# Kernel tuning notes

Measured on AMD Instinct MI355X. Metric: run time of the kernel, lower is better.

Reference implementation:

```python
import jax, jax.numpy as jnp
import numpy as np

N, E, F_IN, ED, G, LAT = 50000, 800000, 16, 4, 500, 32
HID = 64
EPS = 1e-5
NEG = 0.2


def _gat(x, src, dst, ea, W, a_s, a_d, We, a_e, bias, heads, ch):
    n = x.shape[0]
    h = (x @ W).reshape(n, heads, ch)                      # [N,H,C]
    he = (ea @ We).reshape(-1, heads, ch)                  # [E,H,C]
    asrc = jnp.sum(h * a_s, -1)                            # [N,H]
    adst = jnp.sum(h * a_d, -1)                            # [N,H]
    ae = jnp.sum(he * a_e, -1)                             # [E,H]
    alpha = jax.nn.leaky_relu(asrc[src] + adst[dst] + ae, NEG)
    amax = jax.ops.segment_max(alpha, dst, num_segments=n)
    amax = jnp.where(jnp.isfinite(amax), amax, 0.0)
    ealpha = jnp.exp(alpha - amax[dst])
    denom = jax.ops.segment_sum(ealpha, dst, num_segments=n)
    coef = ealpha / (denom[dst] + 1e-16)                   # [E,H]
    msg = h[src] * coef[:, :, None]                        # [E,H,C]
    out = jax.ops.segment_sum(msg, dst, num_segments=n)
    return out.reshape(n, heads * ch) + bias


def _bn(x, g, b):
    mu = x.mean(0)
    var = x.var(0)
    return g * (x - mu) * jax.lax.rsqrt(var + EPS) + b


def setup_inputs():
    key = jax.random.key(0)
    ks = jax.random.split(key, 20)
    d = {}
    d['x'] = jax.random.normal(ks[0], (N, F_IN), jnp.float32)
    d['edge_index'] = jax.random.randint(ks[1], (2, E), 0, N, jnp.int32)
    d['edge_attr'] = jax.random.normal(ks[2], (E, ED), jnp.float32)
    d['batch'] = jnp.sort(jax.random.randint(ks[3], (N,), 0, G, jnp.int32))
    d['W1'] = jax.random.normal(ks[4], (F_IN, 3 * HID), jnp.float32) / np.sqrt(F_IN)
    d['a1s'] = jax.random.normal(ks[5], (3, HID), jnp.float32) / np.sqrt(HID)
    d['a1d'] = jax.random.normal(ks[6], (3, HID), jnp.float32) / np.sqrt(HID)
    d['We1'] = jax.random.normal(ks[7], (ED, 3 * HID), jnp.float32) / np.sqrt(ED)
    d['a1e'] = jax.random.normal(ks[8], (3, HID), jnp.float32) / np.sqrt(HID)
    d['b1'] = jnp.zeros((3 * HID,), jnp.float32)
    d['g1'] = jnp.ones((3 * HID,), jnp.float32)
    d['be1'] = jnp.zeros((3 * HID,), jnp.float32)
    d['W2'] = jax.random.normal(ks[9], (3 * HID, HID), jnp.float32) / np.sqrt(3 * HID)
    d['a2s'] = jax.random.normal(ks[10], (1, HID), jnp.float32) / np.sqrt(HID)
    d['a2d'] = jax.random.normal(ks[11], (1, HID), jnp.float32) / np.sqrt(HID)
    d['We2'] = jax.random.normal(ks[12], (ED, HID), jnp.float32) / np.sqrt(ED)
    d['a2e'] = jax.random.normal(ks[13], (1, HID), jnp.float32) / np.sqrt(HID)
    d['b2'] = jnp.zeros((HID,), jnp.float32)
    d['g2'] = jnp.ones((HID,), jnp.float32)
    d['be2'] = jnp.zeros((HID,), jnp.float32)
    d['wA'] = jax.random.normal(ks[14], (HID, 1), jnp.float32) / np.sqrt(HID)
    d['bA'] = jnp.zeros((1,), jnp.float32)
    d['wMu'] = jax.random.normal(ks[15], (HID, LAT), jnp.float32) / np.sqrt(HID)
    d['bMu'] = jnp.zeros((LAT,), jnp.float32)
    d['wLv'] = jax.random.normal(ks[16], (HID, LAT), jnp.float32) / np.sqrt(HID)
    d['bLv'] = jnp.zeros((LAT,), jnp.float32)
    return d


def reference(x, edge_index, edge_attr, batch, W1, a1s, a1d, We1, a1e, b1, g1, be1,
              W2, a2s, a2d, We2, a2e, b2, g2, be2, wA, bA, wMu, bMu, wLv, bLv):
    src, dst = edge_index[0], edge_index[1]
    h1 = _gat(x, src, dst, edge_attr, W1, a1s, a1d, We1, a1e, b1, 3, HID)
    h1 = _bn(jax.nn.elu(h1), g1, be1)
    h2 = _gat(h1, src, dst, edge_attr, W2, a2s, a2d, We2, a2e, b2, 1, HID)
    h2 = _bn(jax.nn.elu(h2), g2, be2)
    gate = jax.nn.sigmoid(h2 @ wA + bA)                    # [N,1]
    h2 = h2 * gate
    hg = jax.ops.segment_sum(h2, batch, num_segments=G)    # [G,HID]
    return hg @ wMu + bMu, hg @ wLv + bLv
```

## Files before the change

kernel.cpp:

```cpp
#include <hip/hip_runtime.h>
#include <math.h>

#define N_NODES 50000
#define N_EDGES 800000
#define FIN     16
#define EDIM    4
#define NGRAPH  500
#define LATD    32
#define HID     64
#define C1      192
#define H1      3
#define EPS_BN  1e-5f
#define NEGSL   0.2f
#define ROWS1   128
#define ROWS2   128
#define PAD2    196

__device__ __forceinline__ float wred(float v) {
    #pragma unroll
    for (int o = 32; o > 0; o >>= 1) v += __shfl_xor(v, o, 64);
    return v;
}
__device__ __forceinline__ float wmax(float v) {
    #pragma unroll
    for (int o = 32; o > 0; o >>= 1) v = fmaxf(v, __shfl_xor(v, o, 64));
    return v;
}

__global__ void k_v(const float* __restrict__ We1, const float* __restrict__ a1e,
                    const float* __restrict__ We2, const float* __restrict__ a2e,
                    float* __restrict__ V) {
    int t = threadIdx.x;
    if (t < 12) {
        int k = t / 3, h = t % 3;
        float s = 0.f;
        for (int c = 0; c < HID; ++c) s += We1[k*C1 + h*HID + c] * a1e[h*HID + c];
        V[k*3 + h] = s;
    } else if (t < 16) {
        int k = t - 12;
        float s = 0.f;
        for (int c = 0; c < HID; ++c) s += We2[k*HID + c] * a2e[c];
        V[12 + k] = s;
    }
}

__global__ void k_h1att(const float* __restrict__ x, const float* __restrict__ W1,
                        const float* __restrict__ a1s, const float* __restrict__ a1d,
                        float* __restrict__ h1, float* __restrict__ asrc,
                        float* __restrict__ adst) {
    int w = blockIdx.x * (blockDim.x >> 6) + (threadIdx.x >> 6);
    int lane = threadIdx.x & 63;
    if (w >= N_NODES * H1) return;
    int n = w / H1, h = w % H1;
    int c = h*HID + lane;
    const float* xr = x + n * FIN;
    float acc = 0.f;
    #pragma unroll
    for (int k = 0; k < FIN; ++k) acc += xr[k] * W1[k*C1 + c];
    h1[n*C1 + c] = acc;
    float s = wred(acc * a1s[c]);
    float d = wred(acc * a1d[c]);
    if (lane == 0) { asrc[n*H1 + h] = s; adst[n*H1 + h] = d; }
}

__global__ void k_deg(const int* __restrict__ ei, int* __restrict__ deg) {
    int e = blockIdx.x * blockDim.x + threadIdx.x;
    if (e >= N_EDGES) return;
    atomicAdd(&deg[ei[N_EDGES + e]], 1);
}

__global__ void k_scan(const int* __restrict__ deg, int* __restrict__ row,
                       int* __restrict__ cur) {
    __shared__ int part[1024];
    const int T = 1024, CH = 52;
    int t = threadIdx.x;
    int base = t * CH;
    int s = 0;
    if (base < N_NODES) {
        int hi = min(base + CH, N_NODES);
        int i = base;
        for (; i + 3 < hi; i += 4) { int4 v = *(const int4*)(deg + i); s += v.x + v.y + v.z + v.w; }
        for (; i < hi; ++i) s += deg[i];
    }
    part[t] = s;
    __syncthreads();
    for (int off = 1; off < T; off <<= 1) {
        int v = (t >= off) ? part[t - off] : 0;
        __syncthreads();
        part[t] += v;
        __syncthreads();
    }
    int run = (t == 0) ? 0 : part[t - 1];
    if (base <= N_NODES) {
        int hi = min(base + CH, N_NODES + 1);
        for (int i = base; i < hi; ++i) {
            row[i] = run;
            if (i < N_NODES) { cur[i] = run; run += deg[i]; }
        }
    }
}

__global__ void k_perm(const int* __restrict__ ei, int* __restrict__ cur,
                       int* __restrict__ eperm) {
    int e = blockIdx.x * blockDim.x + threadIdx.x;
    if (e >= N_EDGES) return;
    int d = ei[N_EDGES + e];
    int j = atomicAdd(&cur[d], 1);
    eperm[j] = e;
}

__global__ void k_fill2(const int* __restrict__ ei, const float* __restrict__ ea,
                        const int* __restrict__ eperm,
                        const float* __restrict__ asrc, const float* __restrict__ adst,
                        const float* __restrict__ V,
                        int* __restrict__ srcp, int* __restrict__ dstp,
                        float* __restrict__ alpha1, float* __restrict__ ae2) {
    int j = blockIdx.x * blockDim.x + threadIdx.x;
    if (j >= N_EDGES) return;
    int e = eperm[j];
    int s = ei[e], d = ei[N_EDGES + e];
    srcp[j] = s;
    dstp[j] = d;
    float4 ev = ((const float4*)ea)[e];
    ae2[j] = ev.x*V[12] + ev.y*V[13] + ev.z*V[14] + ev.w*V[15];
    #pragma unroll
    for (int h = 0; h < H1; ++h) {
        float a = asrc[s*H1 + h] + adst[d*H1 + h]
                + ev.x*V[h] + ev.y*V[3+h] + ev.z*V[6+h] + ev.w*V[9+h];
        a = a > 0.f ? a : NEGSL * a;
        alpha1[(size_t)h*N_EDGES + j] = a;
    }
}

__global__ void k_agg1(const int* __restrict__ row, const int* __restrict__ srcp,
                       const float* __restrict__ alpha, const float* __restrict__ h1,
                       float* __restrict__ out1) {
    __shared__ int2 pairs[4][64];
    int wid = threadIdx.x >> 6;
    int lane = threadIdx.x & 63;
    int w = blockIdx.x * 4 + wid;
    if (w >= N_NODES * H1) return;
    int d = w / H1, h = w % H1;
    int r0 = row[d], r1 = row[d + 1];
    const float* ap = alpha + (size_t)h*N_EDGES;

    float m = -1e30f;
    for (int j = r0 + lane; j < r1; j += 64) m = fmaxf(m, ap[j]);
    m = wmax(m);

    float ssum = 0.f;
    for (int j = r0 + lane; j < r1; j += 64) ssum += __expf(ap[j] - m);
    ssum = wred(ssum);
    float inv = 1.f / (ssum + 1e-16f);

    int slot = lane >> 4, c4 = lane & 15;
    const float* hbase = h1 + h*HID + c4*4;
    float4 acc = make_float4(0.f, 0.f, 0.f, 0.f);
    for (int base = r0; base < r1; base += 64) {
        int n = min(64, r1 - base);
        if (lane < n) {
            float cf = __expf(ap[base + lane] - m) * inv;
            pairs[wid][lane] = make_int2(srcp[base + lane], __float_as_int(cf));
        }
        #pragma unroll 4
        for (int idx = slot; idx < n; idx += 4) {
            int2 p = pairs[wid][idx];
            float cf = __int_as_float(p.y);
            const float4 hv = *(const float4*)(hbase + (size_t)p.x * C1);
            acc.x += cf * hv.x; acc.y += cf * hv.y;
            acc.z += cf * hv.z; acc.w += cf * hv.w;
        }
    }
    #pragma unroll
    for (int o = 16; o < 64; o <<= 1) {
        acc.x += __shfl_xor(acc.x, o, 64);
        acc.y += __shfl_xor(acc.y, o, 64);
        acc.z += __shfl_xor(acc.z, o, 64);
        acc.w += __shfl_xor(acc.w, o, 64);
    }
    if (lane < 16)
        *(float4*)(out1 + (size_t)d*C1 + h*HID + c4*4) = acc;
}

__global__ void k_stats1(float* __restrict__ out, const float* __restrict__ b,
                         float* __restrict__ stats) {
    int c = threadIdx.x;
    int r0 = blockIdx.x * ROWS1;
    int r1 = min(r0 + ROWS1, N_NODES);
    float bc = b[c];
    float s = 0.f, ss = 0.f;
    for (int r = r0; r < r1; ++r) {
        float v = out[r*C1 + c] + bc;
        v = v > 0.f ? v : expm1f(v);
        out[r*C1 + c] = v;
        s += v; ss += v * v;
    }
    atomicAdd(&stats[c], s);
    atomicAdd(&stats[C1 + c], ss);
}

__global__ void k_fin1(float* __restrict__ stats) {
    int c = threadIdx.x;
    if (c < C1) {
        float mu  = stats[c] / (float)N_NODES;
        float var = stats[C1 + c] / (float)N_NODES - mu * mu;
        stats[2*C1 + c] = mu;
        stats[3*C1 + c] = rsqrtf(var + EPS_BN);
    }
}

__global__ void k_norm1(float* __restrict__ out, const float* __restrict__ g,
                        const float* __restrict__ be, const float* __restrict__ stats) {
    int i = blockIdx.x * blockDim.x + threadIdx.x;
    if (i >= N_NODES * C1) return;
    int c = i % C1;
    out[i] = g[c] * (out[i] - stats[2*C1 + c]) * stats[3*C1 + c] + be[c];
}

__global__ void __launch_bounds__(256) k_h2(
        const float* __restrict__ h1bn, const float* __restrict__ W2,
        const float* __restrict__ a2s, const float* __restrict__ a2d,
        float* __restrict__ h2, float* __restrict__ asrc, float* __restrict__ adst) {
    __shared__ float As[64 * PAD2];
    int tid = threadIdx.x;
    int nb = blockIdx.x * 64;
    const float4* src = (const float4*)(h1bn + (size_t)nb * C1);
    #pragma unroll
    for (int j = 0; j < 12; ++j) {
        int idx = tid + j * 256;
        int n = idx / 48, kq = idx - n * 48;
        *(float4*)(As + n * PAD2 + kq * 4) = src[idx];
    }
    __syncthreads();

    int lane = tid & 63;
    int tx = lane & 15, tyw = lane >> 4;
    int ty = (tid >> 6) * 4 + tyw;
    int r0 = ty * 4;
    const float* wp = W2 + tx * 4;

    float4 acc0 = {0,0,0,0}, acc1 = {0,0,0,0}, acc2 = {0,0,0,0}, acc3 = {0,0,0,0};
    #pragma unroll 4
    for (int k = 0; k < C1; ++k) {
        float4 w4 = *(const float4*)(wp + k * HID);
        float a0 = As[(r0+0)*PAD2 + k];
        float a1 = As[(r0+1)*PAD2 + k];
        float a2 = As[(r0+2)*PAD2 + k];
        float a3 = As[(r0+3)*PAD2 + k];
        acc0.x += a0*w4.x; acc0.y += a0*w4.y; acc0.z += a0*w4.z; acc0.w += a0*w4.w;
        acc1.x += a1*w4.x; acc1.y += a1*w4.y; acc1.z += a1*w4.z; acc1.w += a1*w4.w;
        acc2.x += a2*w4.x; acc2.y += a2*w4.y; acc2.z += a2*w4.z; acc2.w += a2*w4.w;
        acc3.x += a3*w4.x; acc3.y += a3*w4.y; acc3.z += a3*w4.z; acc3.w += a3*w4.w;
    }

    float4 s4 = *(const float4*)(a2s + tx*4);
    float4 d4 = *(const float4*)(a2d + tx*4);

    #define H2_EPI(ACC, I)                                                        \
    {                                                                             \
        int n = nb + r0 + (I);                                                    \
        float s = ACC.x*s4.x + ACC.y*s4.y + ACC.z*s4.z + ACC.w*s4.w;              \
        float d = ACC.x*d4.x + ACC.y*d4.y + ACC.z*d4.z + ACC.w*d4.w;              \
        s += __shfl_xor(s, 1, 64); s += __shfl_xor(s, 2, 64);                     \
        s += __shfl_xor(s, 4, 64); s += __shfl_xor(s, 8, 64);                     \
        d += __shfl_xor(d, 1, 64); d += __shfl_xor(d, 2, 64);                     \
        d += __shfl_xor(d, 4, 64); d += __shfl_xor(d, 8, 64);                     \
        if (n < N_NODES) {                                                        \
            *(float4*)(h2 + (size_t)n*HID + tx*4) = ACC;                          \
            if (tx == 0) { asrc[n] = s; adst[n] = d; }                            \
        }                                                                         \
    }
    H2_EPI(acc0, 0)
    H2_EPI(acc1, 1)
    H2_EPI(acc2, 2)
    H2_EPI(acc3, 3)
    #undef H2_EPI
}

__global__ void k_alpha2(const int* __restrict__ srcp, const int* __restrict__ dstp,
                         const float* __restrict__ ae2,
                         const float* __restrict__ asrc, const float* __restrict__ adst,
                         float* __restrict__ alpha2) {
    int j = blockIdx.x * blockDim.x + threadIdx.x;
    if (j >= N_EDGES) return;
    float a = asrc[srcp[j]] + adst[dstp[j]] + ae2[j];
    a = a > 0.f ? a : NEGSL * a;
    alpha2[j] = a;
}

__global__ void k_agg2(const int* __restrict__ row, const int* __restrict__ srcp,
                       const float* __restrict__ alpha, const float* __restrict__ h2,
                       float* __restrict__ out2) {
    __shared__ int2 pairs[4][64];
    int wid = threadIdx.x >> 6;
    int lane = threadIdx.x & 63;
    int d = blockIdx.x * 4 + wid;
    if (d >= N_NODES) return;
    int r0 = row[d], r1 = row[d + 1];

    float m = -1e30f;
    for (int j = r0 + lane; j < r1; j += 64) m = fmaxf(m, alpha[j]);
    m = wmax(m);

    float ssum = 0.f;
    for (int j = r0 + lane; j < r1; j += 64) ssum += __expf(alpha[j] - m);
    ssum = wred(ssum);
    float inv = 1.f / (ssum + 1e-16f);

    int slot = lane >> 4, c4 = lane & 15;
    const float* hbase = h2 + c4*4;
    float4 acc = make_float4(0.f, 0.f, 0.f, 0.f);
    for (int base = r0; base < r1; base += 64) {
        int n = min(64, r1 - base);
        if (lane < n) {
            float cf = __expf(alpha[base + lane] - m) * inv;
            pairs[wid][lane] = make_int2(srcp[base + lane], __float_as_int(cf));
        }
        #pragma unroll 4
        for (int idx = slot; idx < n; idx += 4) {
            int2 p = pairs[wid][idx];
            float cf = __int_as_float(p.y);
            const float4 hv = *(const float4*)(hbase + (size_t)p.x * HID);
            acc.x += cf * hv.x; acc.y += cf * hv.y;
            acc.z += cf * hv.z; acc.w += cf * hv.w;
        }
    }
    #pragma unroll
    for (int o = 16; o < 64; o <<= 1) {
        acc.x += __shfl_xor(acc.x, o, 64);
        acc.y += __shfl_xor(acc.y, o, 64);
        acc.z += __shfl_xor(acc.z, o, 64);
        acc.w += __shfl_xor(acc.w, o, 64);
    }
    if (lane < 16)
        *(float4*)(out2 + (size_t)d*HID + c4*4) = acc;
}

__global__ void k_stats2(float* __restrict__ out, const float* __restrict__ b,
                         float* __restrict__ stats) {
    int c = threadIdx.x & 63;
    int rep = threadIdx.x >> 6;
    int base = blockIdx.x * ROWS2;
    int r1 = min(base + ROWS2, N_NODES);
    float bc = b[c];
    float s = 0.f, ss = 0.f;
    for (int r = base + rep; r < r1; r += 4) {
        float v = out[r*HID + c] + bc;
        v = v > 0.f ? v : expm1f(v);
        out[r*HID + c] = v;
        s += v; ss += v * v;
    }
    __shared__ float ls[256], lss[256];
    ls[threadIdx.x] = s; lss[threadIdx.x] = ss;
    __syncthreads();
    if (rep == 0) {
        s  = ls[c]  + ls[64+c]  + ls[128+c]  + ls[192+c];
        ss = lss[c] + lss[64+c] + lss[128+c] + lss[192+c];
        atomicAdd(&stats[768 + c], s);
        atomicAdd(&stats[832 + c], ss);
    }
}

__global__ void k_fin2(float* __restrict__ stats) {
    int c = threadIdx.x;
    if (c < HID) {
        float mu  = stats[768 + c] / (float)N_NODES;
        float var = stats[832 + c] / (float)N_NODES - mu * mu;
        stats[896 + c] = mu;
        stats[960 + c] = rsqrtf(var + EPS_BN);
    }
}

__global__ void k_final(const float* __restrict__ out2, const float* __restrict__ g,
                        const float* __restrict__ be, const float* __restrict__ stats,
                        const float* __restrict__ wA, const float* __restrict__ bA,
                        const int* __restrict__ batch, float* __restrict__ hg) {
    int n = blockIdx.x * (blockDim.x >> 6) + (threadIdx.x >> 6);
    int lane = threadIdx.x & 63;
    if (n >= N_NODES) return;
    float v = out2[n*HID + lane];
    v = g[lane] * (v - stats[896 + lane]) * stats[960 + lane] + be[lane];
    float gs = wred(v * wA[lane]);
    float gate = 1.f / (1.f + expf(-(gs + bA[0])));
    atomicAdd(&hg[batch[n]*HID + lane], v * gate);
}

__global__ void k_out(const float* __restrict__ hg, const float* __restrict__ wMu,
                      const float* __restrict__ bMu, const float* __restrict__ wLv,
                      const float* __restrict__ bLv, float* __restrict__ out) {
    __shared__ float rowv[HID];
    int gid = blockIdx.x, t = threadIdx.x;
    rowv[t] = hg[gid*HID + t];
    __syncthreads();
    if (t < LATD) {
        float s = 0.f;
        #pragma unroll
        for (int k = 0; k < HID; ++k) s += rowv[k] * wMu[k*LATD + t];
        out[gid*LATD + t] = s + bMu[t];
    } else {
        int c = t - LATD;
        float s = 0.f;
        #pragma unroll
        for (int k = 0; k < HID; ++k) s += rowv[k] * wLv[k*LATD + c];
        out[NGRAPH*LATD + gid*LATD + c] = s + bLv[c];
    }
}

extern "C" void kernel_launch(void* const* d_in, const int* in_sizes, int n_in,
                              void* d_out, int out_size, void* d_ws, size_t ws_size,
                              hipStream_t stream) {
    const float* x   = (const float*)d_in[0];
    const int*   ei  = (const int*)  d_in[1];
    const float* ea  = (const float*)d_in[2];
    const int*   bat = (const int*)  d_in[3];
    const float* W1  = (const float*)d_in[4];
    const float* a1s = (const float*)d_in[5];
    const float* a1d = (const float*)d_in[6];
    const float* We1 = (const float*)d_in[7];
    const float* a1e = (const float*)d_in[8];
    const float* b1  = (const float*)d_in[9];
    const float* g1  = (const float*)d_in[10];
    const float* be1 = (const float*)d_in[11];
    const float* W2  = (const float*)d_in[12];
    const float* a2s = (const float*)d_in[13];
    const float* a2d = (const float*)d_in[14];
    const float* We2 = (const float*)d_in[15];
    const float* a2e = (const float*)d_in[16];
    const float* b2  = (const float*)d_in[17];
    const float* g2  = (const float*)d_in[18];
    const float* be2 = (const float*)d_in[19];
    const float* wA  = (const float*)d_in[20];
    const float* bA  = (const float*)d_in[21];
    const float* wMu = (const float*)d_in[22];
    const float* bMu = (const float*)d_in[23];
    const float* wLv = (const float*)d_in[24];
    const float* bLv = (const float*)d_in[25];
    float* out = (float*)d_out;
    float* w = (float*)d_ws;

    const size_t oH1   = 0;
    const size_t oO1   = oH1  + (size_t)N_NODES*C1;
    const size_t oAS   = oO1  + (size_t)N_NODES*C1;
    const size_t oAD   = oAS  + (size_t)N_NODES*H1;
    const size_t oSRC  = oAD  + (size_t)N_NODES*H1;
    const size_t oDST  = oSRC + (size_t)N_EDGES;
    const size_t oAE2  = oDST + (size_t)N_EDGES;
    const size_t oAL   = oAE2 + (size_t)N_EDGES;
    const size_t oROW  = oAL  + (size_t)N_EDGES*H1;
    const size_t oCUR  = oROW + (size_t)(N_NODES+1);
    const size_t oPERM = oCUR + (size_t)N_NODES;
    const size_t Z0raw = oPERM + (size_t)N_EDGES;
    const size_t Z0    = (Z0raw + 3) & ~(size_t)3;
    const size_t oDEG  = Z0;
    const size_t oST   = oDEG + (size_t)N_NODES;
    const size_t oHG   = oST  + 1024;
    const size_t oV    = oHG  + (size_t)NGRAPH*HID;
    const size_t oEND  = oV   + 64;

    hipMemsetAsync(w + Z0, 0, (oEND - Z0) * sizeof(float), stream);

    k_v<<<1, 64, 0, stream>>>(We1, a1e, We2, a2e, w + oV);
    k_h1att<<<(N_NODES*H1 + 3)/4, 256, 0, stream>>>(x, W1, a1s, a1d,
                                                    w + oH1, w + oAS, w + oAD);
    k_deg<<<(N_EDGES + 255)/256, 256, 0, stream>>>(ei, (int*)(w + oDEG));
    k_scan<<<1, 1024, 0, stream>>>((int*)(w + oDEG), (int*)(w + oROW), (int*)(w + oCUR));
    k_perm<<<(N_EDGES + 255)/256, 256, 0, stream>>>(ei, (int*)(w + oCUR), (int*)(w + oPERM));
    k_fill2<<<(N_EDGES + 255)/256, 256, 0, stream>>>(ei, ea, (int*)(w + oPERM),
                                                     w + oAS, w + oAD, w + oV,
                                                     (int*)(w + oSRC), (int*)(w + oDST),
                                                     w + oAL, w + oAE2);

    k_agg1<<<(N_NODES*H1 + 3)/4, 256, 0, stream>>>((int*)(w + oROW), (int*)(w + oSRC),
                                                   w + oAL, w + oH1, w + oO1);
    k_stats1<<<(N_NODES + ROWS1 - 1)/ROWS1, C1, 0, stream>>>(w + oO1, b1, w + oST);
    k_fin1<<<1, C1, 0, stream>>>(w + oST);
    k_norm1<<<(N_NODES*C1 + 255)/256, 256, 0, stream>>>(w + oO1, g1, be1, w + oST);

    k_h2<<<(N_NODES + 63)/64, 256, 0, stream>>>(w + oO1, W2, a2s, a2d,
                                                w + oH1, w + oAS, w + oAD);
    k_alpha2<<<(N_EDGES + 255)/256, 256, 0, stream>>>((int*)(w + oSRC), (int*)(w + oDST),
                                                      w + oAE2, w + oAS, w + oAD, w + oAL);
    k_agg2<<<(N_NODES + 3)/4, 256, 0, stream>>>((int*)(w + oROW), (int*)(w + oSRC),
                                                w + oAL, w + oH1, w + oO1);
    k_stats2<<<(N_NODES + ROWS2 - 1)/ROWS2, 256, 0, stream>>>(w + oO1, b2, w + oST);
    k_fin2<<<1, HID, 0, stream>>>(w + oST);
    k_final<<<(N_NODES + 3)/4, 256, 0, stream>>>(w + oO1, g2, be2, w + oST, wA, bA, bat, w + oHG);
    k_out<<<NGRAPH, HID, 0, stream>>>(w + oHG, wMu, bMu, wLv, bLv, out);
}
```

Baseline: 670.0 us.

## Replace single-block degree scan with three-phase multi-block scan

The CSR row-offset prefix scan previously ran in one 1024-thread block, with each thread serially walking 52 degrees and using a shared-memory Hillis-Steele scan with many barriers. It is now split into three kernels: per-block reductions over 512-node chunks, a single small block that scans the 98 block sums with wave shuffles, and a per-block wave-shuffle scan that writes row and cur offsets. This spreads the scan across many CUs at the cost of two extra kernel launches and a small amount of extra workspace.

```diff
diff --git a/kernel.cpp b/kernel.cpp
--- a/kernel.cpp
+++ b/kernel.cpp
@@ -15,6 +15,8 @@
 #define ROWS1   128
 #define ROWS2   128
 #define PAD2    196
+#define SCHUNK  512
+#define NSBLK   ((N_NODES + SCHUNK - 1) / SCHUNK)
 
 __device__ __forceinline__ float wred(float v) {
     #pragma unroll
@@ -69,35 +71,62 @@
     atomicAdd(&deg[ei[N_EDGES + e]], 1);
 }
 
-__global__ void k_scan(const int* __restrict__ deg, int* __restrict__ row,
-                       int* __restrict__ cur) {
-    __shared__ int part[1024];
-    const int T = 1024, CH = 52;
+__global__ void k_scanA(const int* __restrict__ deg, int* __restrict__ bsum) {
+    __shared__ int wtot[4];
+    int t = threadIdx.x, b = blockIdx.x;
+    int i0 = b * SCHUNK + t * 2;
+    int v = 0;
+    if (i0 + 1 < N_NODES) { int2 p = *(const int2*)(deg + i0); v = p.x + p.y; }
+    else if (i0 < N_NODES) v = deg[i0];
+    #pragma unroll
+    for (int o = 32; o > 0; o >>= 1) v += __shfl_xor(v, o, 64);
+    if ((t & 63) == 0) wtot[t >> 6] = v;
+    __syncthreads();
+    if (t == 0) bsum[b] = wtot[0] + wtot[1] + wtot[2] + wtot[3];
+}
+
+__global__ void k_scanB(const int* __restrict__ bsum, int* __restrict__ boff,
+                        int* __restrict__ row) {
+    __shared__ int w0tot;
     int t = threadIdx.x;
-    int base = t * CH;
-    int s = 0;
-    if (base < N_NODES) {
-        int hi = min(base + CH, N_NODES);
-        int i = base;
-        for (; i + 3 < hi; i += 4) { int4 v = *(const int4*)(deg + i); s += v.x + v.y + v.z + v.w; }
-        for (; i < hi; ++i) s += deg[i];
-    }
-    part[t] = s;
+    int v = (t < NSBLK) ? bsum[t] : 0;
+    int inc = v;
+    int lane = t & 63;
+    #pragma unroll
+    for (int o = 1; o < 64; o <<= 1) {
+        int n = __shfl_up(inc, o, 64);
+        if (lane >= o) inc += n;
+    }
+    if (t == 63) w0tot = inc;
     __syncthreads();
-    for (int off = 1; off < T; off <<= 1) {
-        int v = (t >= off) ? part[t - off] : 0;
-        __syncthreads();
-        part[t] += v;
-        __syncthreads();
-    }
-    int run = (t == 0) ? 0 : part[t - 1];
-    if (base <= N_NODES) {
-        int hi = min(base + CH, N_NODES + 1);
-        for (int i = base; i < hi; ++i) {
-            row[i] = run;
-            if (i < N_NODES) { cur[i] = run; run += deg[i]; }
-        }
-    }
+    int off = (t >= 64) ? w0tot : 0;
+    if (t < NSBLK) boff[t] = inc - v + off;
+    if (t == 0) row[N_NODES] = N_EDGES;
+}
+
+__global__ void k_scanC(const int* __restrict__ deg, const int* __restrict__ boff,
+                        int* __restrict__ row, int* __restrict__ cur) {
+    __shared__ int wtot[4];
+    int t = threadIdx.x, b = blockIdx.x;
+    int i0 = b * SCHUNK + t * 2;
+    int d0 = 0, d1 = 0;
+    if (i0 + 1 < N_NODES) { int2 p = *(const int2*)(deg + i0); d0 = p.x; d1 = p.y; }
+    else if (i0 < N_NODES) d0 = deg[i0];
+    int ps = d0 + d1;
+    int inc = ps;
+    int lane = t & 63, wid = t >> 6;
+    #pragma unroll
+    for (int o = 1; o < 64; o <<= 1) {
+        int n = __shfl_up(inc, o, 64);
+        if (lane >= o) inc += n;
+    }
+    if (lane == 63) wtot[wid] = inc;
+    __syncthreads();
+    int woff = 0;
+    for (int ww = 0; ww < wid; ++ww) woff += wtot[ww];
+    int ex = boff[b] + woff + inc - ps;
+    if (i0 < N_NODES)     { row[i0]   = ex;      cur[i0]   = ex;      }
+    if (i0 + 1 < N_NODES) { row[i0+1] = ex + d0; cur[i0+1] = ex + d0; }
 }
 
 __global__ void k_perm(const int* __restrict__ ei, int* __restrict__ cur,
@@ -449,7 +478,9 @@
     const size_t oROW  = oAL  + (size_t)N_EDGES*H1;
     const size_t oCUR  = oROW + (size_t)(N_NODES+1);
     const size_t oPERM = oCUR + (size_t)N_NODES;
-    const size_t Z0raw = oPERM + (size_t)N_EDGES;
+    const size_t oBSUM = oPERM+ (size_t)N_EDGES;
+    const size_t oBOFF = oBSUM+ (size_t)NSBLK;
+    const size_t Z0raw = oBOFF+ (size_t)NSBLK;
     const size_t Z0    = (Z0raw + 3) & ~(size_t)3;
     const size_t oDEG  = Z0;
     const size_t oST   = oDEG + (size_t)N_NODES;
@@ -463,7 +494,10 @@
     k_h1att<<<(N_NODES*H1 + 3)/4, 256, 0, stream>>>(x, W1, a1s, a1d,
                                                     w + oH1, w + oAS, w + oAD);
     k_deg<<<(N_EDGES + 255)/256, 256, 0, stream>>>(ei, (int*)(w + oDEG));
-    k_scan<<<1, 1024, 0, stream>>>((int*)(w + oDEG), (int*)(w + oROW), (int*)(w + oCUR));
+    k_scanA<<<NSBLK, 256, 0, stream>>>((int*)(w + oDEG), (int*)(w + oBSUM));
+    k_scanB<<<1, 128, 0, stream>>>((int*)(w + oBSUM), (int*)(w + oBOFF), (int*)(w + oROW));
+    k_scanC<<<NSBLK, 256, 0, stream>>>((int*)(w + oDEG), (int*)(w + oBOFF),
+                                       (int*)(w + oROW), (int*)(w + oCUR));
     k_perm<<<(N_EDGES + 255)/256, 256, 0, stream>>>(ei, (int*)(w + oCUR), (int*)(w + oPERM));
     k_fill2<<<(N_EDGES + 255)/256, 256, 0, stream>>>(ei, ea, (int*)(w + oPERM),
                                                      w + oAS, w + oAD, w + oV,
```

Result: faster. 584.5 us (-12.8%).
